# Kernel optimization log

Hardware: AMD Instinct MI355X
Metric: run time of the kernel (lower is better)

The kernel has to match this reference:

```python
import jax, jax.numpy as jnp
import numpy as np

# Per-sample token counts per octree depth layer (full octree, depth 1..5)
LENS = (8, 64, 512, 4096, 32768)
OFFS = np.concatenate([[0], np.cumsum(LENS)]).astype(int)
CONV = (1, 1, 1, 4, 8)  # conv stride/kernel per layer: basic x3, half-conv (2^(3-1)), single-conv (2^3)
B, E = 8, 256
NUM_VOCAB, RES, SDIM = 16, 32, 3
S = int(OFFS[-1])  # 37448


def setup_inputs() -> dict:
    key = jax.random.key(0)
    ks = jax.random.split(key, 16)
    value = jax.random.randint(ks[0], (B, S), 1, NUM_VOCAB + 1)
    # depth: fixed sorted octree pattern, same for every sample
    depth_row = np.concatenate([np.full(l, d + 1, dtype=np.int64) for d, l in enumerate(LENS)])
    depth = jnp.broadcast_to(jnp.asarray(depth_row), (B, S))
    position = jax.random.randint(ks[1], (B, S, SDIM), 1, 2 * RES)
    sc = 0.02
    val_emb = (jax.random.normal(ks[2], (5, NUM_VOCAB + 1, E)) * sc).at[:, 0].set(0.0)
    dep_emb = (jax.random.normal(ks[3], (5, RES + 1, E)) * sc).at[:, 0].set(0.0)
    pos_emb = (jax.random.normal(ks[4], (5, SDIM, 2 * RES, E)) * sc).at[:, :, 0].set(0.0)
    conv4_w = jax.random.normal(ks[5], (E, E, 4)) * sc
    conv4_b = jax.random.normal(ks[6], (E,)) * sc
    conv8_w = jax.random.normal(ks[7], (E, E, 8)) * sc
    conv8_b = jax.random.normal(ks[8], (E,)) * sc
    return {"value": value, "depth": depth, "position": position,
            "val_emb": val_emb, "dep_emb": dep_emb, "pos_emb": pos_emb,
            "conv4_w": conv4_w, "conv4_b": conv4_b, "conv8_w": conv8_w, "conv8_b": conv8_b}


def _embed(v, d, p, ve, de, pe):
    # sum of value, depth, and per-axis spatial embeddings  [B, L, E]
    return ve[v] + de[d] + pe[0][p[:, :, 0]] + pe[1][p[:, :, 1]] + pe[2][p[:, :, 2]]


def _conv(x, w, b, s):
    # Conv1d(kernel=stride=s) == blockwise GEMM over non-overlapping windows
    Bb, L, Ee = x.shape
    xr = x.reshape(Bb, L // s, s, Ee)
    return jnp.einsum('blki,oik->blo', xr, w) + b


def reference(value, depth, position, val_emb, dep_emb, pos_emb, conv4_w, conv4_b, conv8_w, conv8_b):
    convs = {3: (conv4_w, conv4_b), 4: (conv8_w, conv8_b)}
    outs = []
    for li in range(5):
        s0, s1 = int(OFFS[li]), int(OFFS[li + 1])
        x = _embed(value[:, s0:s1], depth[:, s0:s1], position[:, s0:s1],
                   val_emb[li], dep_emb[li], pos_emb[li])
        if CONV[li] > 1:
            w, b = convs[li]
            x = _conv(x, w, b, CONV[li])
        outs.append(x)
    # all samples share the depth layout -> equal lengths, pad_sequence is a no-op concat
    return jnp.concatenate(outs, axis=1)  # [B, 5704, E]
```

## Files before the change

### kernel.cpp

```cpp
#include <hip/hip_runtime.h>
#include <hip/hip_bf16.h>

#define S_TOT 37448
#define OUT_ROWS 5704
#define EDIM 256
#define BATCH 8

typedef __attribute__((ext_vector_type(8))) short short8;
typedef __attribute__((ext_vector_type(4))) float f32x4;
typedef __attribute__((ext_vector_type(4))) unsigned int u32x4;

__device__ __forceinline__ short f2b(float f) {
    unsigned u = __builtin_bit_cast(unsigned, f);
    unsigned r = (u + 0x7fffu + ((u >> 16) & 1u)) >> 16;
    return (short)r;
}
__device__ __forceinline__ float b2f(short s) {
    unsigned u = ((unsigned)(unsigned short)s) << 16;
    return __builtin_bit_cast(float, u);
}

__device__ __forceinline__ void embed8f(const float* ve, const float* de,
                                        const float* q0, const float* q1, const float* q2,
                                        float* s) {
#pragma unroll
    for (int h = 0; h < 2; ++h) {
        f32x4 a = *(const f32x4*)(ve + h * 4);
        f32x4 b = *(const f32x4*)(de + h * 4);
        f32x4 c = *(const f32x4*)(q0 + h * 4);
        f32x4 d = *(const f32x4*)(q1 + h * 4);
        f32x4 e = *(const f32x4*)(q2 + h * 4);
#pragma unroll
        for (int j = 0; j < 4; ++j)
            s[h * 4 + j] = a[j] + b[j] + c[j] + d[j] + e[j];
    }
}

__device__ __forceinline__ void acc_bf8(float* a, short8 s) {
    u32x4 u = __builtin_bit_cast(u32x4, s);
#pragma unroll
    for (int j = 0; j < 4; ++j) {
        a[2 * j]     += __builtin_bit_cast(float, u[j] << 16);
        a[2 * j + 1] += __builtin_bit_cast(float, u[j] & 0xffff0000u);
    }
}

template <int S>
__device__ __forceinline__ void transform_body(const float* __restrict__ w,
                                               short* __restrict__ dst, int bid, int tid) {
    int idx = bid * 256 + tid;
    int l  = idx & 63;
    int nf = (idx >> 6) & 15;
    int kb = idx >> 10;
    int o = nf * 16 + (l & 15);
    int kap0 = kb * 32 + ((l >> 4) << 3);
    short8 r;
#pragma unroll
    for (int j = 0; j < 8; ++j) {
        int kap = kap0 + j;
        int kpos = kap >> 8;
        int i = kap & 255;
        r[j] = f2b(w[(o * 256 + i) * S + kpos]);
    }
    *(short8*)(dst + idx * 8) = r;
}

__global__ __launch_bounds__(256) void transform_both(
        const float* __restrict__ w4, const float* __restrict__ w8,
        short* __restrict__ wt4, short* __restrict__ wt8) {
    int bid = blockIdx.x, tid = threadIdx.x;
    if (bid < 128) transform_body<4>(w4, wt4, bid, tid);
    else           transform_body<8>(w8, wt8, bid - 128, tid);
}

template <int S>
__device__ __forceinline__ void precompute_body(
        const float* __restrict__ val_emb, const float* __restrict__ dep_emb,
        const float* __restrict__ pos_emb, const short* __restrict__ wt2,
        short* __restrict__ P, int bid, int tid, short* As) {
    constexpr int LI = (S == 4) ? 3 : 4;
    const int lane = tid & 63;
    const int wid = tid >> 6;
    const int wave_m = wid >> 1;
    const int wave_n = wid & 1;
    const int k  = bid >> 2;
    const int mt = bid & 3;

    f32x4 acc[2][8];
#pragma unroll
    for (int i = 0; i < 2; ++i)
#pragma unroll
        for (int j = 0; j < 8; ++j) acc[i][j] = (f32x4){0.f, 0.f, 0.f, 0.f};

    const int tk = tid >> 5;
    const int f0 = (tid & 31) * 8;
    const float* dep = dep_emb + (LI * 33 + LI + 1) * 256;

#pragma unroll
    for (int m8 = 0; m8 < 8; ++m8) {
        int m = m8 * 8 + tk;
        int R = mt * 64 + m;
        short8 r;
        if (R < 17) {
            const float* src = val_emb + (LI * 17 + R) * 256;
#pragma unroll
            for (int j = 0; j < 8; ++j) r[j] = f2b(src[f0 + j] + dep[f0 + j]);
        } else if (R < 209) {
            int ax = (R < 81) ? 0 : (R < 145 ? 1 : 2);
            int rr = R - (ax == 0 ? 17 : (ax == 1 ? 81 : 145));
            const float* src = pos_emb + ((LI * 3 + ax) * 64 + rr) * 256;
#pragma unroll
            for (int j = 0; j < 8; ++j) r[j] = f2b(src[f0 + j]);
        } else {
            r = (short8){0, 0, 0, 0, 0, 0, 0, 0};
        }
        int byte = (m * 512 + f0 * 2) ^ ((m & 7) << 4);
        *(short8*)((char*)As + byte) = r;
    }
    __syncthreads();

#pragma unroll
    for (int ks = 0; ks < 8; ++ks) {
        short8 af[2];
#pragma unroll
        for (int mf = 0; mf < 2; ++mf) {
            int m = wave_m * 32 + mf * 16 + (lane & 15);
            int byte = (m * 512 + ks * 64 + ((lane >> 4) << 4)) ^ ((m & 7) << 4);
            af[mf] = *(const short8*)((const char*)As + byte);
        }
        int kbg = k * 8 + ks;
#pragma unroll
        for (int nf = 0; nf < 8; ++nf) {
            int nfg = wave_n * 8 + nf;
            short8 bfr = *(const short8*)(wt2 + ((kbg * 16 + nfg) * 64 + lane) * 8);
            acc[0][nf] = __builtin_amdgcn_mfma_f32_16x16x32_bf16(af[0], bfr, acc[0][nf], 0, 0, 0);
            acc[1][nf] = __builtin_amdgcn_mfma_f32_16x16x32_bf16(af[1], bfr, acc[1][nf], 0, 0, 0);
        }
    }

#pragma unroll
    for (int mf = 0; mf < 2; ++mf) {
#pragma unroll
        for (int nf = 0; nf < 8; ++nf) {
            int n = wave_n * 128 + nf * 16 + (lane & 15);
            int r0 = mt * 64 + wave_m * 32 + mf * 16 + ((lane >> 4) << 2);
#pragma unroll
            for (int reg = 0; reg < 4; ++reg)
                P[(k * 256 + r0 + reg) * 256 + n] = f2b(acc[mf][nf][reg]);
        }
    }
}

__global__ __launch_bounds__(256) void precompute_both(
        const float* __restrict__ val_emb, const float* __restrict__ dep_emb,
        const float* __restrict__ pos_emb, const short* __restrict__ wt4,
        const short* __restrict__ wt8, short* __restrict__ P4, short* __restrict__ P8) {
    __shared__ __align__(16) short As[64 * 256];
    if (blockIdx.x < 16)
        precompute_body<4>(val_emb, dep_emb, pos_emb, wt4, P4, blockIdx.x, threadIdx.x, As);
    else
        precompute_body<8>(val_emb, dep_emb, pos_emb, wt8, P8, blockIdx.x - 16, threadIdx.x, As);
}

template <int S>
__device__ __forceinline__ void gather_body(
        const int* __restrict__ value, const int* __restrict__ position,
        const short* __restrict__ P, const float* __restrict__ bias,
        float* __restrict__ out, int bid, int tid, int4* idx_lds) {
    constexpr int L_OUT = (S == 4) ? 1024 : 4096;
    constexpr int OFF_IN = (S == 4) ? 584 : 4680;
    constexpr int OFF_OUT = (S == 4) ? 584 : 1608;

    const int R0 = bid * 8;
    if (tid < 8 * S) {
        int r = tid / S, k = tid - r * S;
        int R = R0 + r;
        int b = R / L_OUT, l = R - b * L_OUT;
        int t = b * S_TOT + OFF_IN + l * S + k;
        int v = value[t];
        const int* pp = position + t * 3;
        idx_lds[r * S + k] = make_int4(v << 8, (17 + pp[0]) << 8,
                                       (81 + pp[1]) << 8, (145 + pp[2]) << 8);
    }
    __syncthreads();

    const int r = tid >> 5;
    const int og = (tid & 31) * 8;
    const int R = R0 + r;
    const int b = R / L_OUT, l = R - b * L_OUT;

    float a[8];
    f32x4 b0 = *(const f32x4*)(bias + og);
    f32x4 b1 = *(const f32x4*)(bias + og + 4);
#pragma unroll
    for (int j = 0; j < 4; ++j) { a[j] = b0[j]; a[4 + j] = b1[j]; }

    const short* Pg = P + og;
#pragma unroll
    for (int k = 0; k < S; ++k) {
        int4 id = idx_lds[r * S + k];
        const short* Pk = Pg + (k << 16);
        short8 s0 = *(const short8*)(Pk + id.x);
        short8 s1 = *(const short8*)(Pk + id.y);
        short8 s2 = *(const short8*)(Pk + id.z);
        short8 s3 = *(const short8*)(Pk + id.w);
        acc_bf8(a, s0);
        acc_bf8(a, s1);
        acc_bf8(a, s2);
        acc_bf8(a, s3);
    }

    float* op = out + ((long)b * OUT_ROWS + OFF_OUT + l) * EDIM + og;
    *(f32x4*)op = (f32x4){a[0], a[1], a[2], a[3]};
    *(f32x4*)(op + 4) = (f32x4){a[4], a[5], a[6], a[7]};
}

__device__ __forceinline__ void embed_small_body(
        const int* __restrict__ value, const int* __restrict__ depth,
        const int* __restrict__ position, const float* __restrict__ val_emb,
        const float* __restrict__ dep_emb, const float* __restrict__ pos_emb,
        float* __restrict__ out, int bid, int tid) {
    int idx = bid * 256 + tid;
    int token = idx >> 5;
    int f0 = (idx & 31) * 8;
    int b = token / 584;
    int r = token - b * 584;
    int li = (r < 8) ? 0 : (r < 72 ? 1 : 2);
    int base = b * S_TOT + r;
    int v = value[base];
    int d = depth[base];
    const int* pp = position + base * 3;
    const float* ve = val_emb + ((li * 17 + v) << 8) + f0;
    const float* de = dep_emb + ((li * 33 + d) << 8) + f0;
    const float* q0 = pos_emb + (((li * 3 + 0) * 64 + pp[0]) << 8) + f0;
    const float* q1 = pos_emb + (((li * 3 + 1) * 64 + pp[1]) << 8) + f0;
    const float* q2 = pos_emb + (((li * 3 + 2) * 64 + pp[2]) << 8) + f0;
    float s[8];
    embed8f(ve, de, q0, q1, q2, s);
    float* op = out + ((long)b * OUT_ROWS + r) * EDIM + f0;
    *(f32x4*)op = (f32x4){s[0], s[1], s[2], s[3]};
    *(f32x4*)(op + 4) = (f32x4){s[4], s[5], s[6], s[7]};
}

__global__ __launch_bounds__(256) void gather_mega(
        const int* __restrict__ value, const int* __restrict__ depth,
        const int* __restrict__ position, const float* __restrict__ val_emb,
        const float* __restrict__ dep_emb, const float* __restrict__ pos_emb,
        const short* __restrict__ P4, const short* __restrict__ P8,
        const float* __restrict__ b4, const float* __restrict__ b8,
        float* __restrict__ out) {
    __shared__ int4 idx_lds[64];
    int bid = blockIdx.x, tid = threadIdx.x;
    if (bid < 4096)
        gather_body<8>(value, position, P8, b8, out, bid, tid, idx_lds);
    else if (bid < 5120)
        gather_body<4>(value, position, P4, b4, out, bid - 4096, tid, idx_lds);
    else
        embed_small_body(value, depth, position, val_emb, dep_emb, pos_emb, out, bid - 5120, tid);
}

template <int S>
__global__ __launch_bounds__(256) void conv_kernel(
        const int* __restrict__ value, const int* __restrict__ depth,
        const int* __restrict__ position, const float* __restrict__ val_emb,
        const float* __restrict__ dep_emb, const float* __restrict__ pos_emb,
        const short* __restrict__ wt2, const float* __restrict__ bias,
        float* __restrict__ out) {
    constexpr int LI = (S == 4) ? 3 : 4;
    constexpr int L_OUT = (S == 4) ? 1024 : 4096;
    constexpr int OFF_IN = (S == 4) ? 584 : 4680;
    constexpr int OFF_OUT = (S == 4) ? 584 : 1608;

    __shared__ __align__(16) short As[64 * 256];

    const int tid = threadIdx.x;
    const int lane = tid & 63;
    const int wid = tid >> 6;
    const int wave_m = wid >> 1;
    const int wave_n = wid & 1;
    const int mg0 = blockIdx.x * 64;
    const int b = mg0 / L_OUT;
    const int l0 = mg0 - b * L_OUT;

    f32x4 acc[2][8];
#pragma unroll
    for (int i = 0; i < 2; ++i)
#pragma unroll
        for (int j = 0; j < 8; ++j) acc[i][j] = (f32x4){0.f, 0.f, 0.f, 0.f};

    const int tk = tid >> 5;
    const int f0 = (tid & 31) * 8;

    for (int cp = 0; cp < S; ++cp) {
        __syncthreads();
#pragma unroll
        for (int m8 = 0; m8 < 8; ++m8) {
            int m = m8 * 8 + tk;
            int t = OFF_IN + (l0 + m) * S + cp;
            int base = b * S_TOT + t;
            int v = value[base];
            int d = depth[base];
            const int* pp = position + base * 3;
            const float* ve = val_emb + ((LI * 17 + v) << 8) + f0;
            const float* de = dep_emb + ((LI * 33 + d) << 8) + f0;
            const float* q0 = pos_emb + (((LI * 3 + 0) * 64 + pp[0]) << 8) + f0;
            const float* q1 = pos_emb + (((LI * 3 + 1) * 64 + pp[1]) << 8) + f0;
            const float* q2 = pos_emb + (((LI * 3 + 2) * 64 + pp[2]) << 8) + f0;
            float s[8];
            embed8f(ve, de, q0, q1, q2, s);
            short8 r;
#pragma unroll
            for (int j = 0; j < 8; ++j) r[j] = f2b(s[j]);
            int byte = (m * 512 + f0 * 2) ^ ((m & 7) << 4);
            *(short8*)((char*)As + byte) = r;
        }
        __syncthreads();
#pragma unroll
        for (int ks = 0; ks < 8; ++ks) {
            short8 af[2];
#pragma unroll
            for (int mf = 0; mf < 2; ++mf) {
                int m = wave_m * 32 + mf * 16 + (lane & 15);
                int byte = (m * 512 + ks * 64 + ((lane >> 4) << 4)) ^ ((m & 7) << 4);
                af[mf] = *(const short8*)((const char*)As + byte);
            }
            int kbg = cp * 8 + ks;
#pragma unroll
            for (int nf = 0; nf < 8; ++nf) {
                int nfg = wave_n * 8 + nf;
                short8 bfr = *(const short8*)(wt2 + ((kbg * 16 + nfg) * 64 + lane) * 8);
                acc[0][nf] = __builtin_amdgcn_mfma_f32_16x16x32_bf16(af[0], bfr, acc[0][nf], 0, 0, 0);
                acc[1][nf] = __builtin_amdgcn_mfma_f32_16x16x32_bf16(af[1], bfr, acc[1][nf], 0, 0, 0);
            }
        }
    }

#pragma unroll
    for (int mf = 0; mf < 2; ++mf) {
#pragma unroll
        for (int nf = 0; nf < 8; ++nf) {
            int n = wave_n * 128 + nf * 16 + (lane & 15);
            float bv = bias[n];
            int r0 = l0 + wave_m * 32 + mf * 16 + ((lane >> 4) << 2);
#pragma unroll
            for (int reg = 0; reg < 4; ++reg)
                out[((long)b * OUT_ROWS + OFF_OUT + r0 + reg) * EDIM + n] =
                    acc[mf][nf][reg] + bv;
        }
    }
}

__global__ __launch_bounds__(256) void embed_small_kernel(
        const int* __restrict__ value, const int* __restrict__ depth,
        const int* __restrict__ position, const float* __restrict__ val_emb,
        const float* __restrict__ dep_emb, const float* __restrict__ pos_emb,
        float* __restrict__ out) {
    embed_small_body(value, depth, position, val_emb, dep_emb, pos_emb, out,
                     blockIdx.x, threadIdx.x);
}

extern "C" void kernel_launch(void* const* d_in, const int* in_sizes, int n_in,
                              void* d_out, int out_size, void* d_ws, size_t ws_size,
                              hipStream_t stream) {
    const int* value = (const int*)d_in[0];
    const int* depth = (const int*)d_in[1];
    const int* position = (const int*)d_in[2];
    const float* val_emb = (const float*)d_in[3];
    const float* dep_emb = (const float*)d_in[4];
    const float* pos_emb = (const float*)d_in[5];
    const float* w4 = (const float*)d_in[6];
    const float* b4 = (const float*)d_in[7];
    const float* w8 = (const float*)d_in[8];
    const float* b8 = (const float*)d_in[9];
    float* out = (float*)d_out;

    short* wt4 = (short*)d_ws;
    short* wt8 = wt4 + 262144;
    short* P4  = (short*)((char*)d_ws + 1572864);
    short* P8  = P4 + 262144;
    const size_t need = 3145728;

    transform_both<<<dim3(384), dim3(256), 0, stream>>>(w4, w8, wt4, wt8);

    if (ws_size >= need) {
        precompute_both<<<dim3(48), dim3(256), 0, stream>>>(val_emb, dep_emb, pos_emb,
                                                            wt4, wt8, P4, P8);
        gather_mega<<<dim3(5704), dim3(256), 0, stream>>>(value, depth, position,
                                                          val_emb, dep_emb, pos_emb,
                                                          P4, P8, b4, b8, out);
    } else {
        embed_small_kernel<<<dim3(584), dim3(256), 0, stream>>>(value, depth, position,
                                                                val_emb, dep_emb, pos_emb, out);
        conv_kernel<4><<<dim3(128), dim3(256), 0, stream>>>(value, depth, position, val_emb,
                                                            dep_emb, pos_emb, wt4, b4, out);
        conv_kernel<8><<<dim3(512), dim3(256), 0, stream>>>(value, depth, position, val_emb,
                                                            dep_emb, pos_emb, wt8, b8, out);
    }
}
```

Baseline: 62.42 us.

## Fuse weight bf16 transform into precompute GEMM and prefetch gather loads

Removes the separate weight transform kernel on the fast path: the precompute GEMM now reads fp32 conv weights directly with strided loads and converts them to bf16 in registers. This saves one launch and a workspace round trip, at the cost of uncoalesced strided global reads inside the MFMA loop. The gather loop is also software-pipelined so the next kernel position's four table rows load while the current ones accumulate.

```diff
diff --git a/kernel.cpp b/kernel.cpp
--- a/kernel.cpp
+++ b/kernel.cpp
@@ -46,37 +46,9 @@
 }
 
 template <int S>
-__device__ __forceinline__ void transform_body(const float* __restrict__ w,
-                                               short* __restrict__ dst, int bid, int tid) {
-    int idx = bid * 256 + tid;
-    int l  = idx & 63;
-    int nf = (idx >> 6) & 15;
-    int kb = idx >> 10;
-    int o = nf * 16 + (l & 15);
-    int kap0 = kb * 32 + ((l >> 4) << 3);
-    short8 r;
-#pragma unroll
-    for (int j = 0; j < 8; ++j) {
-        int kap = kap0 + j;
-        int kpos = kap >> 8;
-        int i = kap & 255;
-        r[j] = f2b(w[(o * 256 + i) * S + kpos]);
-    }
-    *(short8*)(dst + idx * 8) = r;
-}
-
-__global__ __launch_bounds__(256) void transform_both(
-        const float* __restrict__ w4, const float* __restrict__ w8,
-        short* __restrict__ wt4, short* __restrict__ wt8) {
-    int bid = blockIdx.x, tid = threadIdx.x;
-    if (bid < 128) transform_body<4>(w4, wt4, bid, tid);
-    else           transform_body<8>(w8, wt8, bid - 128, tid);
-}
-
-template <int S>
 __device__ __forceinline__ void precompute_body(
         const float* __restrict__ val_emb, const float* __restrict__ dep_emb,
-        const float* __restrict__ pos_emb, const short* __restrict__ wt2,
+        const float* __restrict__ pos_emb, const float* __restrict__ w,
         short* __restrict__ P, int bid, int tid, short* As) {
     constexpr int LI = (S == 4) ? 3 : 4;
     const int lane = tid & 63;
@@ -128,11 +100,14 @@
             int byte = (m * 512 + ks * 64 + ((lane >> 4) << 4)) ^ ((m & 7) << 4);
             af[mf] = *(const short8*)((const char*)As + byte);
         }
-        int kbg = k * 8 + ks;
+        const int ib = ks * 32 + ((lane >> 4) << 3);
 #pragma unroll
         for (int nf = 0; nf < 8; ++nf) {
             int nfg = wave_n * 8 + nf;
-            short8 bfr = *(const short8*)(wt2 + ((kbg * 16 + nfg) * 64 + lane) * 8);
+            const float* wb = w + ((long)((nfg * 16 + (lane & 15)) * 256 + ib)) * S + k;
+            short8 bfr;
+#pragma unroll
+            for (int j = 0; j < 8; ++j) bfr[j] = f2b(wb[j * S]);
             acc[0][nf] = __builtin_amdgcn_mfma_f32_16x16x32_bf16(af[0], bfr, acc[0][nf], 0, 0, 0);
             acc[1][nf] = __builtin_amdgcn_mfma_f32_16x16x32_bf16(af[1], bfr, acc[1][nf], 0, 0, 0);
         }
@@ -151,15 +126,15 @@
     }
 }
 
-__global__ __launch_bounds__(256) void precompute_both(
+__global__ __launch_bounds__(256) void precompute_fused(
         const float* __restrict__ val_emb, const float* __restrict__ dep_emb,
-        const float* __restrict__ pos_emb, const short* __restrict__ wt4,
-        const short* __restrict__ wt8, short* __restrict__ P4, short* __restrict__ P8) {
+        const float* __restrict__ pos_emb, const float* __restrict__ w4,
+        const float* __restrict__ w8, short* __restrict__ P4, short* __restrict__ P8) {
     __shared__ __align__(16) short As[64 * 256];
     if (blockIdx.x < 16)
-        precompute_body<4>(val_emb, dep_emb, pos_emb, wt4, P4, blockIdx.x, threadIdx.x, As);
+        precompute_body<4>(val_emb, dep_emb, pos_emb, w4, P4, blockIdx.x, threadIdx.x, As);
     else
-        precompute_body<8>(val_emb, dep_emb, pos_emb, wt8, P8, blockIdx.x - 16, threadIdx.x, As);
+        precompute_body<8>(val_emb, dep_emb, pos_emb, w8, P8, blockIdx.x - 16, threadIdx.x, As);
 }
 
 template <int S>
@@ -196,18 +171,27 @@
     for (int j = 0; j < 4; ++j) { a[j] = b0[j]; a[4 + j] = b1[j]; }
 
     const short* Pg = P + og;
+    int4 id0 = idx_lds[r * S];
+    short8 s0 = *(const short8*)(Pg + id0.x);
+    short8 s1 = *(const short8*)(Pg + id0.y);
+    short8 s2 = *(const short8*)(Pg + id0.z);
+    short8 s3 = *(const short8*)(Pg + id0.w);
 #pragma unroll
     for (int k = 0; k < S; ++k) {
-        int4 id = idx_lds[r * S + k];
-        const short* Pk = Pg + (k << 16);
-        short8 s0 = *(const short8*)(Pk + id.x);
-        short8 s1 = *(const short8*)(Pk + id.y);
-        short8 s2 = *(const short8*)(Pk + id.z);
-        short8 s3 = *(const short8*)(Pk + id.w);
+        short8 t0 = s0, t1 = s1, t2 = s2, t3 = s3;
+        if (k + 1 < S) {
+            int4 idn = idx_lds[r * S + k + 1];
+            const short* Pn = Pg + ((k + 1) << 16);
+            t0 = *(const short8*)(Pn + idn.x);
+            t1 = *(const short8*)(Pn + idn.y);
+            t2 = *(const short8*)(Pn + idn.z);
+            t3 = *(const short8*)(Pn + idn.w);
+        }
         acc_bf8(a, s0);
         acc_bf8(a, s1);
         acc_bf8(a, s2);
         acc_bf8(a, s3);
+        s0 = t0; s1 = t1; s2 = t2; s3 = t3;
     }
 
     float* op = out + ((long)b * OUT_ROWS + OFF_OUT + l) * EDIM + og;
@@ -260,6 +244,43 @@
 }
 
 template <int S>
+__device__ __forceinline__ void transform_body(const float* __restrict__ w,
+                                               short* __restrict__ dst, int bid, int tid) {
+    int idx = bid * 256 + tid;
+    int l  = idx & 63;
+    int nf = (idx >> 6) & 15;
+    int kb = idx >> 10;
+    int o = nf * 16 + (l & 15);
+    int kap0 = kb * 32 + ((l >> 4) << 3);
+    short8 r;
+#pragma unroll
+    for (int j = 0; j < 8; ++j) {
+        int kap = kap0 + j;
+        int kpos = kap >> 8;
+        int i = kap & 255;
+        r[j] = f2b(w[(o * 256 + i) * S + kpos]);
+    }
+    *(short8*)(dst + idx * 8) = r;
+}
+
+__global__ __launch_bounds__(256) void transform_both(
+        const float* __restrict__ w4, const float* __restrict__ w8,
+        short* __restrict__ wt4, short* __restrict__ wt8) {
+    int bid = blockIdx.x, tid = threadIdx.x;
+    if (bid < 128) transform_body<4>(w4, wt4, bid, tid);
+    else           transform_body<8>(w8, wt8, bid - 128, tid);
+}
+
+__global__ __launch_bounds__(256) void embed_small_kernel(
+        const int* __restrict__ value, const int* __restrict__ depth,
+        const int* __restrict__ position, const float* __restrict__ val_emb,
+        const float* __restrict__ dep_emb, const float* __restrict__ pos_emb,
+        float* __restrict__ out) {
+    embed_small_body(value, depth, position, val_emb, dep_emb, pos_emb, out,
+                     blockIdx.x, threadIdx.x);
+}
+
+template <int S>
 __global__ __launch_bounds__(256) void conv_kernel(
         const int* __restrict__ value, const int* __restrict__ depth,
         const int* __restrict__ position, const float* __restrict__ val_emb,
@@ -350,15 +371,6 @@
     }
 }
 
-__global__ __launch_bounds__(256) void embed_small_kernel(
-        const int* __restrict__ value, const int* __restrict__ depth,
-        const int* __restrict__ position, const float* __restrict__ val_emb,
-        const float* __restrict__ dep_emb, const float* __restrict__ pos_emb,
-        float* __restrict__ out) {
-    embed_small_body(value, depth, position, val_emb, dep_emb, pos_emb, out,
-                     blockIdx.x, threadIdx.x);
-}
-
 extern "C" void kernel_launch(void* const* d_in, const int* in_sizes, int n_in,
                               void* d_out, int out_size, void* d_ws, size_t ws_size,
                               hipStream_t stream) {
@@ -374,21 +386,20 @@
     const float* b8 = (const float*)d_in[9];
     float* out = (float*)d_out;
 
-    short* wt4 = (short*)d_ws;
-    short* wt8 = wt4 + 262144;
-    short* P4  = (short*)((char*)d_ws + 1572864);
-    short* P8  = P4 + 262144;
-    const size_t need = 3145728;
-
-    transform_both<<<dim3(384), dim3(256), 0, stream>>>(w4, w8, wt4, wt8);
+    const size_t need = 1572864;
 
     if (ws_size >= need) {
-        precompute_both<<<dim3(48), dim3(256), 0, stream>>>(val_emb, dep_emb, pos_emb,
-                                                            wt4, wt8, P4, P8);
+        short* P4 = (short*)d_ws;
+        short* P8 = P4 + 262144;
+        precompute_fused<<<dim3(48), dim3(256), 0, stream>>>(val_emb, dep_emb, pos_emb,
+                                                             w4, w8, P4, P8);
         gather_mega<<<dim3(5704), dim3(256), 0, stream>>>(value, depth, position,
                                                           val_emb, dep_emb, pos_emb,
                                                           P4, P8, b4, b8, out);
     } else {
+        short* wt4 = (short*)d_ws;
+        short* wt8 = wt4 + 262144;
+        transform_both<<<dim3(384), dim3(256), 0, stream>>>(w4, w8, wt4, wt8);
         embed_small_kernel<<<dim3(584), dim3(256), 0, stream>>>(value, depth, position,
                                                                 val_emb, dep_emb, pos_emb, out);
         conv_kernel<4><<<dim3(128), dim3(256), 0, stream>>>(value, depth, position, val_emb,
```

New measurement: 96.14 us. 1.54x slower.
